# Performance work log

Measured on AMD Instinct MI355X. Metric: run time of the kernel, lower is better.

## Reference

```python
import jax, jax.numpy as jnp
import numpy as np
from jax import lax

B, C, H, W = 32, 3, 128, 128
NUM_CLASSES = 101
H2, W2 = H // 2, W // 2
N = H2 * W2                      # 4096 graph nodes


def _grid_graph(h, w):
    """4-neighbor bidirectional grid graph + self loops, with GCN sym-norm coeffs."""
    idx = np.arange(h * w).reshape(h, w)
    src = np.concatenate([idx[:, :-1].ravel(), idx[:, 1:].ravel(),
                          idx[:-1, :].ravel(), idx[1:, :].ravel()])
    dst = np.concatenate([idx[:, 1:].ravel(), idx[:, :-1].ravel(),
                          idx[1:, :].ravel(), idx[:-1, :].ravel()])
    # GCNConv default: add self loops, then D^{-1/2} (A+I) D^{-1/2}
    loop = np.arange(h * w)
    src = np.concatenate([src, loop])
    dst = np.concatenate([dst, loop])
    deg = np.bincount(dst, minlength=h * w).astype(np.float32)
    dinv = 1.0 / np.sqrt(deg)
    norm = dinv[src] * dinv[dst]
    return src.astype(np.int32), dst.astype(np.int32), norm.astype(np.float32)


def setup_inputs() -> dict:
    key = jax.random.key(0)
    ks = jax.random.split(key, 9)
    x = jax.random.normal(ks[0], (B, C, H, W), dtype=jnp.float32)
    conv_w = jax.random.normal(ks[1], (32, C, 3, 3), dtype=jnp.float32) * 0.1
    conv_b = jax.random.normal(ks[2], (32,), dtype=jnp.float32) * 0.01
    gcn_w = jax.random.normal(ks[3], (32, 64), dtype=jnp.float32) * 0.15
    gcn_b = jax.random.normal(ks[4], (64,), dtype=jnp.float32) * 0.01
    fc1_w = jax.random.normal(ks[5], (128, 64 * N), dtype=jnp.float32) * (1.0 / 512.0)
    fc1_b = jax.random.normal(ks[6], (128,), dtype=jnp.float32) * 0.01
    fc2_w = jax.random.normal(ks[7], (NUM_CLASSES, 128), dtype=jnp.float32) * 0.08
    fc2_b = jax.random.normal(ks[8], (NUM_CLASSES,), dtype=jnp.float32) * 0.01
    return {"x": x, "conv_w": conv_w, "conv_b": conv_b, "gcn_w": gcn_w,
            "gcn_b": gcn_b, "fc1_w": fc1_w, "fc1_b": fc1_b,
            "fc2_w": fc2_w, "fc2_b": fc2_b}


def reference(x, conv_w, conv_b, gcn_w, gcn_b, fc1_w, fc1_b, fc2_w, fc2_b):
    # conv1 (3x3, pad=1) + relu + maxpool 2x2
    y = lax.conv_general_dilated(x, conv_w, (1, 1), "SAME",
                                 dimension_numbers=("NCHW", "OIHW", "NCHW"))
    y = jax.nn.relu(y + conv_b[None, :, None, None])
    y = lax.reduce_window(y, -jnp.inf, lax.max, (1, 1, 2, 2), (1, 1, 2, 2), "VALID")
    b, c, h2, w2 = y.shape  # [B, 32, 64, 64]

    # faithful torch x.view(B, -1, 32): raw row-major reinterpretation (NOT transpose)
    xg = y.reshape(b, -1, c)  # [B, N, 32]

    # GCNConv(32 -> 64): linear, then gather -> normalize -> scatter-add
    hfeat = jnp.einsum("bnf,fo->bno", xg, gcn_w)  # [B, N, 64]
    src, dst, norm = _grid_graph(h2, w2)
    src = jnp.asarray(src); dst = jnp.asarray(dst)
    coeff = jnp.asarray(norm, hfeat.dtype)[None, :, None]
    msgs = hfeat[:, src, :] * coeff                      # edge-wise gather
    agg = jnp.zeros_like(hfeat).at[:, dst, :].add(msgs)  # scatter-add
    g = jax.nn.relu(agg + gcn_b)

    # flatten + FCs
    flat = g.reshape(b, -1)  # [B, 64*N]
    f1 = jax.nn.relu(flat @ fc1_w.T + fc1_b)
    return f1 @ fc2_w.T + fc2_b
```

## Files before the change

### kernel.cpp

```cpp
#include <hip/hip_runtime.h>


#define K_FC 262144

__global__ __launch_bounds__(256) void k_conv_pool(
    const float* __restrict__ x, const float* __restrict__ cw,
    const float* __restrict__ cb, float* __restrict__ y)
{
    __shared__ float wl[864];
    __shared__ float tin[3 * 34 * 36];

    int blk = blockIdx.x;
    int b = blk >> 4;
    int tile = blk & 15;
    int ph0 = (tile >> 2) << 4;
    int pw0 = (tile & 3) << 4;
    int t = threadIdx.x;

    for (int i = t; i < 864; i += 256) wl[i] = cw[i];

    int r0 = ph0 * 2 - 1;
    int c0 = pw0 * 2 - 1;
    for (int i = t; i < 3 * 34 * 34; i += 256) {
        int ci = i / 1156;
        int rem = i - ci * 1156;
        int yy = rem / 34;
        int xx = rem - yy * 34;
        int gr = r0 + yy, gc = c0 + xx;
        float v = 0.f;
        if (gr >= 0 && gr < 128 && gc >= 0 && gc < 128)
            v = x[((b * 3 + ci) * 128 + gr) * 128 + gc];
        tin[ci * 1224 + yy * 36 + xx] = v;
    }
    __syncthreads();

    int ph = t >> 4, pw = t & 15;
    float p[3][4][4];
#pragma unroll
    for (int ci = 0; ci < 3; ++ci)
#pragma unroll
        for (int dy = 0; dy < 4; ++dy) {
            const float2* row = (const float2*)&tin[ci * 1224 + (2 * ph + dy) * 36 + 2 * pw];
            float2 v0 = row[0], v1 = row[1];
            p[ci][dy][0] = v0.x; p[ci][dy][1] = v0.y;
            p[ci][dy][2] = v1.x; p[ci][dy][3] = v1.y;
        }

    int obase = (b * 32 * 64 + (ph0 + ph)) * 64 + pw0 + pw;
    for (int co = 0; co < 32; ++co) {
        float s00 = 0.f, s01 = 0.f, s10 = 0.f, s11 = 0.f;
#pragma unroll
        for (int ci = 0; ci < 3; ++ci)
#pragma unroll
            for (int ky = 0; ky < 3; ++ky)
#pragma unroll
                for (int kx = 0; kx < 3; ++kx) {
                    float wv = wl[co * 27 + ci * 9 + ky * 3 + kx];
                    s00 = fmaf(p[ci][ky][kx],         wv, s00);
                    s01 = fmaf(p[ci][ky][kx + 1],     wv, s01);
                    s10 = fmaf(p[ci][ky + 1][kx],     wv, s10);
                    s11 = fmaf(p[ci][ky + 1][kx + 1], wv, s11);
                }
        float m = fmaxf(fmaxf(s00, s01), fmaxf(s10, s11)) + cb[co];
        y[obase + co * 4096] = fmaxf(m, 0.f);
    }
}

__device__ __forceinline__ float dinvf(int h, int w) {
    int d = 1 + (w > 0) + (w < 63) + (h > 0) + (h < 63);
    return rsqrtf((float)d);
}

__device__ __forceinline__ void acc4(const float* __restrict__ yb, int hq, int wq,
                                     int fh, float c,
                                     float4& a0, float4& a1, float4& a2, float4& a3)
{
    const float4* s = (const float4*)(yb + (((hq << 6) + wq) << 5) + fh);
    float4 v0 = s[0], v1 = s[1], v2 = s[2], v3 = s[3];
    a0.x = fmaf(c, v0.x, a0.x); a0.y = fmaf(c, v0.y, a0.y);
    a0.z = fmaf(c, v0.z, a0.z); a0.w = fmaf(c, v0.w, a0.w);
    a1.x = fmaf(c, v1.x, a1.x); a1.y = fmaf(c, v1.y, a1.y);
    a1.z = fmaf(c, v1.z, a1.z); a1.w = fmaf(c, v1.w, a1.w);
    a2.x = fmaf(c, v2.x, a2.x); a2.y = fmaf(c, v2.y, a2.y);
    a2.z = fmaf(c, v2.z, a2.z); a2.w = fmaf(c, v2.w, a2.w);
    a3.x = fmaf(c, v3.x, a3.x); a3.y = fmaf(c, v3.y, a3.y);
    a3.z = fmaf(c, v3.z, a3.z); a3.w = fmaf(c, v3.w, a3.w);
}

__global__ __launch_bounds__(256) void k_gcn(
    const float* __restrict__ y, const float* __restrict__ gw,
    const float* __restrict__ gb, float* __restrict__ g)
{
    __shared__ float zl[32 * 132];
    __shared__ float wl[32 * 64];
    __shared__ float bl[64];

    int blk = blockIdx.x;
    int b = blk >> 5;
    int r = blk & 31;
    int t = threadIdx.x;
    const float* yb = y + b * 131072;

    for (int i = t; i < 512; i += 256) ((float4*)wl)[i] = ((const float4*)gw)[i];
    if (t < 64) bl[t] = gb[t];

    {
        int l = t >> 1;
        int fh = (t & 1) << 4;
        int h = 2 * r + (l >> 6);
        int wq = l & 63;
        float dp = dinvf(h, wq);
        float4 a0 = {0,0,0,0}, a1 = {0,0,0,0}, a2 = {0,0,0,0}, a3 = {0,0,0,0};
        acc4(yb, h, wq, fh, dp * dp, a0, a1, a2, a3);
        if (wq > 0)  acc4(yb, h, wq - 1, fh, dp * dinvf(h, wq - 1), a0, a1, a2, a3);
        if (wq < 63) acc4(yb, h, wq + 1, fh, dp * dinvf(h, wq + 1), a0, a1, a2, a3);
        if (h > 0)   acc4(yb, h - 1, wq, fh, dp * dinvf(h - 1, wq), a0, a1, a2, a3);
        if (h < 63)  acc4(yb, h + 1, wq, fh, dp * dinvf(h + 1, wq), a0, a1, a2, a3);
        zl[(fh + 0)  * 132 + l] = a0.x; zl[(fh + 1)  * 132 + l] = a0.y;
        zl[(fh + 2)  * 132 + l] = a0.z; zl[(fh + 3)  * 132 + l] = a0.w;
        zl[(fh + 4)  * 132 + l] = a1.x; zl[(fh + 5)  * 132 + l] = a1.y;
        zl[(fh + 6)  * 132 + l] = a1.z; zl[(fh + 7)  * 132 + l] = a1.w;
        zl[(fh + 8)  * 132 + l] = a2.x; zl[(fh + 9)  * 132 + l] = a2.y;
        zl[(fh + 10) * 132 + l] = a2.z; zl[(fh + 11) * 132 + l] = a2.w;
        zl[(fh + 12) * 132 + l] = a3.x; zl[(fh + 13) * 132 + l] = a3.y;
        zl[(fh + 14) * 132 + l] = a3.z; zl[(fh + 15) * 132 + l] = a3.w;
    }
    __syncthreads();

    int fg = t & 7;
    int ng = t >> 3;
    int n0 = ng << 2;
    int f0 = fg << 3;

    float acc[4][8];
#pragma unroll
    for (int i = 0; i < 4; ++i)
#pragma unroll
        for (int jj = 0; jj < 8; ++jj) acc[i][jj] = 0.f;

#pragma unroll 8
    for (int k = 0; k < 32; ++k) {
        float4 zv  = *(const float4*)&zl[k * 132 + n0];
        float4 wv0 = *(const float4*)&wl[(k << 6) + f0];
        float4 wv1 = *(const float4*)&wl[(k << 6) + f0 + 4];
        float zs[4] = {zv.x, zv.y, zv.z, zv.w};
        float ws[8] = {wv0.x, wv0.y, wv0.z, wv0.w, wv1.x, wv1.y, wv1.z, wv1.w};
#pragma unroll
        for (int i = 0; i < 4; ++i)
#pragma unroll
            for (int jj = 0; jj < 8; ++jj)
                acc[i][jj] = fmaf(zs[i], ws[jj], acc[i][jj]);
    }

    int pbase = r * 128;
    float* gout = g + (size_t)b * 262144;
#pragma unroll
    for (int i = 0; i < 4; ++i) {
        float4 o0, o1;
        o0.x = fmaxf(acc[i][0] + bl[f0 + 0], 0.f);
        o0.y = fmaxf(acc[i][1] + bl[f0 + 1], 0.f);
        o0.z = fmaxf(acc[i][2] + bl[f0 + 2], 0.f);
        o0.w = fmaxf(acc[i][3] + bl[f0 + 3], 0.f);
        o1.x = fmaxf(acc[i][4] + bl[f0 + 4], 0.f);
        o1.y = fmaxf(acc[i][5] + bl[f0 + 5], 0.f);
        o1.z = fmaxf(acc[i][6] + bl[f0 + 6], 0.f);
        o1.w = fmaxf(acc[i][7] + bl[f0 + 7], 0.f);
        float* op = gout + (size_t)(pbase + n0 + i) * 64 + f0;
        *(float4*)op = o0;
        *(float4*)(op + 4) = o1;
    }
}

__global__ __launch_bounds__(256, 3) void k_fc1(
    const float* __restrict__ flat, const float* __restrict__ w,
    float* __restrict__ partial)
{
    __shared__ float Al[32 * 264];

    int t = threadIdx.x;
    int blk = blockIdx.x;
    int k0 = blk << 8;

#pragma unroll
    for (int rr = 0; rr < 8; ++rr) {
        int idx = (rr << 8) + t;
        int b = idx >> 6;
        int c4 = (idx & 63) << 2;
        *(float4*)&Al[b * 264 + c4] =
            *(const float4*)(flat + (size_t)b * K_FC + k0 + c4);
    }
    __syncthreads();

    int s = t & 3;
    int j2 = t >> 2;
    const float* wr0 = w + (size_t)j2 * K_FC + k0 + (s << 2);
    const float* wr1 = wr0 + (size_t)64 * K_FC;

    float acc0[32], acc1[32];
#pragma unroll
    for (int b = 0; b < 32; ++b) { acc0[b] = 0.f; acc1[b] = 0.f; }

#pragma unroll 2
    for (int q = 0; q < 16; ++q) {
        float4 wa = *(const float4*)(wr0 + (q << 4));
        float4 wb = *(const float4*)(wr1 + (q << 4));
        int kk = (q << 4) + (s << 2);
#pragma unroll
        for (int b = 0; b < 32; ++b) {
            float4 a = *(const float4*)&Al[b * 264 + kk];
            acc0[b] = fmaf(a.x, wa.x, acc0[b]);
            acc0[b] = fmaf(a.y, wa.y, acc0[b]);
            acc0[b] = fmaf(a.z, wa.z, acc0[b]);
            acc0[b] = fmaf(a.w, wa.w, acc0[b]);
            acc1[b] = fmaf(a.x, wb.x, acc1[b]);
            acc1[b] = fmaf(a.y, wb.y, acc1[b]);
            acc1[b] = fmaf(a.z, wb.z, acc1[b]);
            acc1[b] = fmaf(a.w, wb.w, acc1[b]);
        }
    }

#pragma unroll
    for (int b = 0; b < 32; ++b) {
        acc0[b] += __shfl_xor(acc0[b], 1);
        acc0[b] += __shfl_xor(acc0[b], 2);
        acc1[b] += __shfl_xor(acc1[b], 1);
        acc1[b] += __shfl_xor(acc1[b], 2);
    }

    float* pout = partial + ((size_t)blk << 12);
#pragma unroll
    for (int i = 0; i < 8; ++i) {
        int b = (s << 3) + i;
        pout[b * 128 + j2]      = acc0[b];
        pout[b * 128 + j2 + 64] = acc1[b];
    }
}

__global__ __launch_bounds__(256) void k_red(
    const float* __restrict__ partial, float* __restrict__ f1)
{
    __shared__ float4 Sl[256];
    int t = threadIdx.x;
    int e4 = (blockIdx.x << 2) + (t & 3);
    int ng = t >> 2;
    const float4* p = (const float4*)partial;
    float4 a = {0.f, 0.f, 0.f, 0.f};
#pragma unroll
    for (int i = 0; i < 16; ++i) {
        int ns = ng + (i << 6);
        float4 v = p[(size_t)ns * 1024 + e4];
        a.x += v.x; a.y += v.y; a.z += v.z; a.w += v.w;
    }
    Sl[t] = a;
    __syncthreads();
    for (int off = 128; off >= 4; off >>= 1) {
        if (t < off) {
            float4 u = Sl[t], v = Sl[t + off];
            u.x += v.x; u.y += v.y; u.z += v.z; u.w += v.w;
            Sl[t] = u;
        }
        __syncthreads();
    }
    if (t < 4) ((float4*)f1)[(blockIdx.x << 2) + t] = Sl[t];
}

__global__ __launch_bounds__(256) void k_fc2(
    const float* __restrict__ f1, const float* __restrict__ b1,
    const float* __restrict__ w2, const float* __restrict__ b2,
    float* __restrict__ out)
{
    int idx = blockIdx.x * 256 + threadIdx.x;
    if (idx >= 32 * 101) return;
    int b = idx / 101;
    int c = idx - b * 101;
    const float4* fp = (const float4*)(f1 + b * 128);
    const float4* bp = (const float4*)b1;
    const float4* wp = (const float4*)(w2 + c * 128);
    float acc = b2[c];
#pragma unroll
    for (int q = 0; q < 32; ++q) {
        float4 f = fp[q], bb = bp[q], ww = wp[q];
        acc = fmaf(fmaxf(f.x + bb.x, 0.f), ww.x, acc);
        acc = fmaf(fmaxf(f.y + bb.y, 0.f), ww.y, acc);
        acc = fmaf(fmaxf(f.z + bb.z, 0.f), ww.z, acc);
        acc = fmaf(fmaxf(f.w + bb.w, 0.f), ww.w, acc);
    }
    out[idx] = acc;
}

extern "C" void kernel_launch(void* const* d_in, const int* in_sizes, int n_in,
                              void* d_out, int out_size, void* d_ws, size_t ws_size,
                              hipStream_t stream)
{
    const float* x  = (const float*)d_in[0];
    const float* cw = (const float*)d_in[1];
    const float* cb = (const float*)d_in[2];
    const float* gw = (const float*)d_in[3];
    const float* gb = (const float*)d_in[4];
    const float* w1 = (const float*)d_in[5];
    const float* b1 = (const float*)d_in[6];
    const float* w2 = (const float*)d_in[7];
    const float* b2 = (const float*)d_in[8];
    float* out = (float*)d_out;

    float* y       = (float*)d_ws;
    float* g       = y + 4194304;
    float* partial = g + 8388608;
    float* f1      = partial + 4194304;

    k_conv_pool<<<512, 256, 0, stream>>>(x, cw, cb, y);
    k_gcn<<<1024, 256, 0, stream>>>(y, gw, gb, g);
    k_fc1<<<1024, 256, 0, stream>>>(g, w1, partial);
    k_red<<<256, 256, 0, stream>>>(partial, f1);
    k_fc2<<<13, 256, 0, stream>>>(f1, b1, w2, b2, out);
}
```

Measured before the change: 282.8 us.

## Retile fc1 register blocking to 8x8 and read conv weights directly

The fc1 split-K kernel changes each thread's register tile from 2 output rows x 32 batches to 8 output rows x 8 batches. This cuts LDS activation reads per FMA by four, at the cost of four thread groups in a block loading the same weight rows, which the cache has to absorb. Partial results are now written as float4 stores, and the occupancy hint rises from 3 to 4 blocks. The conv kernel stops staging its weights in shared memory and reads them from global memory. Those addresses are uniform across the block, so the compiler can likely use scalar loads.

```diff
diff --git a/kernel.cpp b/kernel.cpp
--- a/kernel.cpp
+++ b/kernel.cpp
@@ -7,7 +7,6 @@
     const float* __restrict__ x, const float* __restrict__ cw,
     const float* __restrict__ cb, float* __restrict__ y)
 {
-    __shared__ float wl[864];
     __shared__ float tin[3 * 34 * 36];
 
     int blk = blockIdx.x;
@@ -16,8 +15,6 @@
     int ph0 = (tile >> 2) << 4;
     int pw0 = (tile & 3) << 4;
     int t = threadIdx.x;
-
-    for (int i = t; i < 864; i += 256) wl[i] = cw[i];
 
     int r0 = ph0 * 2 - 1;
     int c0 = pw0 * 2 - 1;
@@ -48,6 +45,7 @@
 
     int obase = (b * 32 * 64 + (ph0 + ph)) * 64 + pw0 + pw;
     for (int co = 0; co < 32; ++co) {
+        const float* wc = cw + co * 27;
         float s00 = 0.f, s01 = 0.f, s10 = 0.f, s11 = 0.f;
 #pragma unroll
         for (int ci = 0; ci < 3; ++ci)
@@ -55,7 +53,7 @@
             for (int ky = 0; ky < 3; ++ky)
 #pragma unroll
                 for (int kx = 0; kx < 3; ++kx) {
-                    float wv = wl[co * 27 + ci * 9 + ky * 3 + kx];
+                    float wv = wc[ci * 9 + ky * 3 + kx];
                     s00 = fmaf(p[ci][ky][kx],         wv, s00);
                     s01 = fmaf(p[ci][ky][kx + 1],     wv, s01);
                     s10 = fmaf(p[ci][ky + 1][kx],     wv, s10);
@@ -171,7 +169,7 @@
     }
 }
 
-__global__ __launch_bounds__(256, 3) void k_fc1(
+__global__ __launch_bounds__(256, 4) void k_fc1(
     const float* __restrict__ flat, const float* __restrict__ w,
     float* __restrict__ partial)
 {
@@ -191,48 +189,56 @@
     }
     __syncthreads();
 
-    int s = t & 3;
-    int j2 = t >> 2;
-    const float* wr0 = w + (size_t)j2 * K_FC + k0 + (s << 2);
-    const float* wr1 = wr0 + (size_t)64 * K_FC;
-
-    float acc0[32], acc1[32];
-#pragma unroll
-    for (int b = 0; b < 32; ++b) { acc0[b] = 0.f; acc1[b] = 0.f; }
-
-#pragma unroll 2
+    int s  = t & 3;
+    int jg = (t >> 2) & 15;
+    int bg = t >> 6;
+    int b0 = bg << 3;
+    int j0 = jg << 3;
+
+    const float* wbase = w + (size_t)j0 * K_FC + k0 + (s << 2);
+
+    float acc[8][8];
+#pragma unroll
+    for (int jj = 0; jj < 8; ++jj)
+#pragma unroll
+        for (int b = 0; b < 8; ++b) acc[jj][b] = 0.f;
+
     for (int q = 0; q < 16; ++q) {
-        float4 wa = *(const float4*)(wr0 + (q << 4));
-        float4 wb = *(const float4*)(wr1 + (q << 4));
+        float4 wv[8];
+#pragma unroll
+        for (int jj = 0; jj < 8; ++jj)
+            wv[jj] = *(const float4*)(wbase + (size_t)jj * K_FC + (q << 4));
         int kk = (q << 4) + (s << 2);
 #pragma unroll
-        for (int b = 0; b < 32; ++b) {
-            float4 a = *(const float4*)&Al[b * 264 + kk];
-            acc0[b] = fmaf(a.x, wa.x, acc0[b]);
-            acc0[b] = fmaf(a.y, wa.y, acc0[b]);
-            acc0[b] = fmaf(a.z, wa.z, acc0[b]);
-            acc0[b] = fmaf(a.w, wa.w, acc0[b]);
-            acc1[b] = fmaf(a.x, wb.x, acc1[b]);
-            acc1[b] = fmaf(a.y, wb.y, acc1[b]);
-            acc1[b] = fmaf(a.z, wb.z, acc1[b]);
-            acc1[b] = fmaf(a.w, wb.w, acc1[b]);
+        for (int b = 0; b < 8; ++b) {
+            float4 a = *(const float4*)&Al[(b0 + b) * 264 + kk];
+#pragma unroll
+            for (int jj = 0; jj < 8; ++jj) {
+                acc[jj][b] = fmaf(a.x, wv[jj].x, acc[jj][b]);
+                acc[jj][b] = fmaf(a.y, wv[jj].y, acc[jj][b]);
+                acc[jj][b] = fmaf(a.z, wv[jj].z, acc[jj][b]);
+                acc[jj][b] = fmaf(a.w, wv[jj].w, acc[jj][b]);
+            }
         }
     }
 
 #pragma unroll
-    for (int b = 0; b < 32; ++b) {
-        acc0[b] += __shfl_xor(acc0[b], 1);
-        acc0[b] += __shfl_xor(acc0[b], 2);
-        acc1[b] += __shfl_xor(acc1[b], 1);
-        acc1[b] += __shfl_xor(acc1[b], 2);
-    }
+    for (int jj = 0; jj < 8; ++jj)
+#pragma unroll
+        for (int b = 0; b < 8; ++b) {
+            acc[jj][b] += __shfl_xor(acc[jj][b], 1);
+            acc[jj][b] += __shfl_xor(acc[jj][b], 2);
+        }
 
     float* pout = partial + ((size_t)blk << 12);
 #pragma unroll
-    for (int i = 0; i < 8; ++i) {
-        int b = (s << 3) + i;
-        pout[b * 128 + j2]      = acc0[b];
-        pout[b * 128 + j2 + 64] = acc1[b];
+    for (int i = 0; i < 2; ++i) {
+        int b = (s << 1) + i;
+        float4 o0 = {acc[0][b], acc[1][b], acc[2][b], acc[3][b]};
+        float4 o1 = {acc[4][b], acc[5][b], acc[6][b], acc[7][b]};
+        float* op = pout + (b0 + b) * 128 + j0;
+        *(float4*)op = o0;
+        *(float4*)(op + 4) = o1;
     }
 }
 
```

Result: slower. 327.6 us (+15.8%).
